# Kernel optimization log

Measured on AMD Instinct MI355X. Metric: run time of the kernel, lower is better.

Reference implementation:

```python
import jax, jax.numpy as jnp
import numpy as np

N_NODES = 100000
N_EDGES = 400000
IN_DIM, HID, OUT_DIM, NUM_REL = 768, 256, 128, 3


def _init_linear(key, fan_in, fan_out):
    k1, k2 = jax.random.split(key)
    s = 1.0 / np.sqrt(fan_in)
    W = jax.random.uniform(k1, (fan_in, fan_out), jnp.float32, -s, s)
    b = jax.random.uniform(k2, (fan_out,), jnp.float32, -s, s)
    return W, b


def setup_inputs() -> dict:
    key = jax.random.key(0)
    ks = jax.random.split(key, 12)
    x = jax.random.normal(ks[0], (N_NODES, IN_DIM), jnp.float32)
    edge_index = jax.random.randint(ks[1], (2, N_EDGES), 0, N_NODES, jnp.int64 if jax.config.jax_enable_x64 else jnp.int32).astype(jnp.int32)
    edge_type = jax.random.randint(ks[2], (N_EDGES,), 0, NUM_REL).astype(jnp.int32)
    W1, b1 = _init_linear(ks[3], IN_DIM, HID)
    s = 1.0 / np.sqrt(HID)
    conv1_W = jax.random.uniform(ks[4], (NUM_REL, HID, HID), jnp.float32, -s, s)
    conv1_root = jax.random.uniform(ks[5], (HID, HID), jnp.float32, -s, s)
    conv1_bias = jnp.zeros((HID,), jnp.float32)
    conv2_W = jax.random.uniform(ks[6], (NUM_REL, HID, HID), jnp.float32, -s, s)
    conv2_root = jax.random.uniform(ks[7], (HID, HID), jnp.float32, -s, s)
    conv2_bias = jnp.zeros((HID,), jnp.float32)
    W2, b2 = _init_linear(ks[8], HID, OUT_DIM)
    Wc, bc = _init_linear(ks[9], OUT_DIM, 2)
    return {"x": x, "edge_index": edge_index, "edge_type": edge_type,
            "batch_size": 1024,
            "W1": W1, "b1": b1,
            "conv1_W": conv1_W, "conv1_root": conv1_root, "conv1_bias": conv1_bias,
            "conv2_W": conv2_W, "conv2_root": conv2_root, "conv2_bias": conv2_bias,
            "W2": W2, "b2": b2, "Wc": Wc, "bc": bc}


def rgcn_conv(h, src, dst, edge_type, W, root, bias):
    # PyG RGCNConv: mean aggregation per relation + root transform + bias
    n = h.shape[0]
    hs = h[src]                                   # [E, HID] gather
    out = h @ root + bias                         # root/self term
    for r in range(NUM_REL):                      # fixed small relation count
        w = (edge_type == r).astype(h.dtype)      # [E]
        msg = (hs @ W[r]) * w[:, None]            # per-relation transform
        ssum = jax.ops.segment_sum(msg, dst, num_segments=n)
        cnt = jax.ops.segment_sum(w, dst, num_segments=n)
        out = out + ssum / jnp.maximum(cnt, 1.0)[:, None]
    return out


def reference(x, edge_index, edge_type, batch_size,
              W1, b1, conv1_W, conv1_root, conv1_bias,
              conv2_W, conv2_root, conv2_bias, W2, b2, Wc, bc):
    src, dst = edge_index[0], edge_index[1]
    h = jax.nn.relu(x @ W1 + b1)                  # linear1 + ReLU
    h = rgcn_conv(h, src, dst, edge_type, conv1_W, conv1_root, conv1_bias)
    # dropout: identity at inference
    h = rgcn_conv(h, src, dst, edge_type, conv2_W, conv2_root, conv2_bias)
    h = jax.nn.relu(h @ W2 + b2)                  # linear2 + ReLU
    logits = h @ Wc + bc                          # classifier
    return logits[:batch_size]
```

## Files before the change

### kernel.cpp

```cpp
#include <hip/hip_runtime.h>


#define N_NODES 100000
#define N_EDGES 400000
#define IN_DIM  768
#define HID     256
#define OUT_DIM 128
#define NREL    3
#define BATCH   1024
#define KCAT    1024
#define MSGW    768
#define CAP0    32768
#define CAP1    8192
#define ECAP1   32768
#define ECAP2   8192

typedef __attribute__((ext_vector_type(8))) short bf16x8;
typedef __attribute__((ext_vector_type(4))) float f32x4;

static __device__ __forceinline__ int imin(int a, int b) { return a < b ? a : b; }

static __device__ __forceinline__ unsigned short f2bf(float f) {
    union { float f; unsigned int u; } v; v.f = f;
    unsigned int r = v.u + 0x7FFFu + ((v.u >> 16) & 1u);
    return (unsigned short)(r >> 16);
}

__global__ __launch_bounds__(256) void zero_prep(
    uint4* __restrict__ zp, int nz,
    const float* __restrict__ W1,
    const float* __restrict__ c1root, const float* __restrict__ c1W,
    const float* __restrict__ c2root, const float* __restrict__ c2W,
    unsigned short* __restrict__ w1s,
    unsigned short* __restrict__ B1s,
    unsigned short* __restrict__ B2s)
{
    int t = blockIdx.x * blockDim.x + threadIdx.x;
    if (t < nz) { zp[t] = make_uint4(0u, 0u, 0u, 0u); return; }
    int u = t - nz;
    const int P1 = (IN_DIM * HID) / 8;
    const int P2 = (KCAT * HID) / 8;
    unsigned int pk[4];
    if (u < P1) {
        int base = u * 8;
        int j0 = base & 31, c = (base >> 5) & 255, s = base >> 13;
        #pragma unroll
        for (int q = 0; q < 4; q++) {
            unsigned short lo = f2bf(W1[((s * 32 + j0 + 2 * q) << 8) + c]);
            unsigned short hi = f2bf(W1[((s * 32 + j0 + 2 * q + 1) << 8) + c]);
            pk[q] = (unsigned int)lo | ((unsigned int)hi << 16);
        }
        *(uint4*)&w1s[base] = make_uint4(pk[0], pk[1], pk[2], pk[3]);
    } else if (u < P1 + 2 * P2) {
        int which2 = (u - P1) >= P2;
        const float* root = which2 ? c2root : c1root;
        const float* Wr   = which2 ? c2W : c1W;
        unsigned short* dst = which2 ? B2s : B1s;
        int base = ((u - P1) - (which2 ? P2 : 0)) * 8;
        int j0 = base & 31, c = (base >> 5) & 255, s = base >> 13;
        int k0 = s * 32 + j0;
        #pragma unroll
        for (int q = 0; q < 4; q++) {
            int ka = k0 + 2 * q, kb = ka + 1;
            float va = (ka < HID) ? root[(ka << 8) + c] : Wr[((ka - HID) << 8) + c];
            float vb = (kb < HID) ? root[(kb << 8) + c] : Wr[((kb - HID) << 8) + c];
            pk[q] = (unsigned int)f2bf(va) | ((unsigned int)f2bf(vb) << 16);
        }
        *(uint4*)&dst[base] = make_uint4(pk[0], pk[1], pk[2], pk[3]);
    }
}


__global__ void mark1c(const int* __restrict__ ei, int* __restrict__ need1,
                       int* __restrict__ elist2, int* __restrict__ ectr2) {
    int e = blockIdx.x * blockDim.x + threadIdx.x;
    if (e >= N_EDGES) return;
    if (ei[N_EDGES + e] < BATCH) {
        need1[ei[e]] = 1;
        int p = atomicAdd(ectr2, 1);
        if (p < ECAP2) elist2[p] = e;
    }
}

__global__ void mark0c(const int* __restrict__ ei, const int* __restrict__ need1,
                       int* __restrict__ need0,
                       int* __restrict__ elist1, int* __restrict__ ectr1) {
    int e = blockIdx.x * blockDim.x + threadIdx.x;
    if (e >= N_EDGES) return;
    int d = ei[N_EDGES + e];
    if (d < BATCH || need1[d]) {
        need0[ei[e]] = 1;
        int p = atomicAdd(ectr1, 1);
        if (p < ECAP1) elist1[p] = e;
    }
}

__global__ void compact_both(const int* __restrict__ need1, const int* __restrict__ need0,
                             int* __restrict__ idx1, int* __restrict__ map1, int* __restrict__ n1ctr,
                             int* __restrict__ idx0, int* __restrict__ map0, int* __restrict__ n0ctr) {
    int i = blockIdx.x * blockDim.x + threadIdx.x;
    if (i >= N_NODES) return;
    int f1 = (i < BATCH) | need1[i];
    int f0 = f1 | need0[i];
    if (f1) {
        int p = atomicAdd(n1ctr, 1);
        if (p < CAP1) { idx1[p] = i; map1[i] = p; } else map1[i] = -1;
    } else map1[i] = -1;
    if (f0) {
        int p = atomicAdd(n0ctr, 1);
        if (p < CAP0) { idx0[p] = i; map0[i] = p; } else map0[i] = -1;
    } else map0[i] = -1;
}

__global__ void scatter_c(const int* __restrict__ ei, const int* __restrict__ et,
                          const int* __restrict__ elist, const int* __restrict__ ectr, int ecap,
                          const int* __restrict__ mapSrc, const int* __restrict__ mapDst,
                          const float* __restrict__ hsrc,
                          float* __restrict__ Amsg, float* __restrict__ cnt,
                          int cntStride) {
    int g = blockIdx.x * blockDim.x + threadIdx.x;
    int ii = g >> 6, lane = g & 63;
    int n = imin(*ectr, ecap);
    if (ii >= n) return;
    int e = elist[ii];
    int d = ei[N_EDGES + e];
    int row = mapDst ? mapDst[d] : d;
    if (row < 0) return;
    int s = mapSrc[ei[e]];
    if (s < 0) return;
    int r = et[e];
    float4 v = *(const float4*)(hsrc + (size_t)s * HID + lane * 4);
    float* dp = Amsg + (size_t)row * MSGW + (size_t)r * HID + lane * 4;
    atomicAdd(dp + 0, v.x);
    atomicAdd(dp + 1, v.y);
    atomicAdd(dp + 2, v.z);
    atomicAdd(dp + 3, v.w);
    if (lane == 0) atomicAdd(cnt + (size_t)r * cntStride + row, 1.0f);
}

__global__ __launch_bounds__(256) void gemm1_mfma(
    const float* __restrict__ x, const int* __restrict__ idx0,
    const unsigned short* __restrict__ w1s, const float* __restrict__ b1,
    float* __restrict__ h0c, const int* __restrict__ Mptr, int Mcap)
{
    int M = imin(*Mptr, Mcap);
    int bm = blockIdx.x * 64;
    if (bm >= M) return;

    __shared__ unsigned short As[64][40];
    __shared__ unsigned short Bs[256][40];

    int tid = threadIdx.x;
    int w = tid >> 6, lane = tid & 63;
    int l16 = lane & 15, lhi = lane >> 4;

    int ar = tid >> 2, ac = tid & 3;
    int gr = idx0[imin(bm + ar, M - 1)];
    const float* aptr = x + (size_t)gr * IN_DIM + ac * 8;

    f32x4 acc[16];
    #pragma unroll
    for (int i = 0; i < 16; i++) acc[i] = (f32x4)0.0f;

    for (int k0 = 0; k0 < IN_DIM; k0 += 32) {
        float4 a0 = *(const float4*)(aptr + k0);
        float4 a1 = *(const float4*)(aptr + k0 + 4);
        unsigned int p0 = (unsigned int)f2bf(a0.x) | ((unsigned int)f2bf(a0.y) << 16);
        unsigned int p1 = (unsigned int)f2bf(a0.z) | ((unsigned int)f2bf(a0.w) << 16);
        unsigned int p2 = (unsigned int)f2bf(a1.x) | ((unsigned int)f2bf(a1.y) << 16);
        unsigned int p3 = (unsigned int)f2bf(a1.z) | ((unsigned int)f2bf(a1.w) << 16);
        *(uint4*)&As[ar][ac * 8] = make_uint4(p0, p1, p2, p3);

        const uint4* bsrc = (const uint4*)(w1s + ((size_t)(k0 >> 5) * 256 + tid) * 32);
        int bswz = (tid >> 3) & 3;
        uint4 b0 = bsrc[0], b1v = bsrc[1], b2 = bsrc[2], b3 = bsrc[3];
        *(uint4*)&Bs[tid][(0 ^ bswz) * 8] = b0;
        *(uint4*)&Bs[tid][(1 ^ bswz) * 8] = b1v;
        *(uint4*)&Bs[tid][(2 ^ bswz) * 8] = b2;
        *(uint4*)&Bs[tid][(3 ^ bswz) * 8] = b3;
        __syncthreads();

        bf16x8 af = *(bf16x8*)&As[w * 16 + l16][lhi * 8];
        #pragma unroll
        for (int f = 0; f < 16; f++) {
            int col = f * 16 + l16;
            bf16x8 bf = *(bf16x8*)&Bs[col][(lhi ^ ((col >> 3) & 3)) * 8];
            acc[f] = __builtin_amdgcn_mfma_f32_16x16x32_bf16(af, bf, acc[f], 0, 0, 0);
        }
        __syncthreads();
    }

    #pragma unroll
    for (int f = 0; f < 16; f++) {
        int col = f * 16 + l16;
        float bb = b1[col];
        #pragma unroll
        for (int reg = 0; reg < 4; reg++) {
            int row = bm + w * 16 + lhi * 4 + reg;
            if (row < M) h0c[(size_t)row * HID + col] = fmaxf(acc[f][reg] + bb, 0.0f);
        }
    }
}

__global__ __launch_bounds__(256) void conv_mfma(
    const float* __restrict__ hsrc,
    const int* __restrict__ idx, const int* __restrict__ map,
    const float* __restrict__ Amsg,
    const float* __restrict__ cnt, int cntStride,
    const unsigned short* __restrict__ Bt, const float* __restrict__ bias,
    float* __restrict__ Cout, const int* __restrict__ Mptr, int Mcap)
{
    int M = Mptr ? imin(*Mptr, Mcap) : Mcap;
    int bm = blockIdx.x * 64;
    if (bm >= M) return;

    __shared__ unsigned short As[64][40];
    __shared__ unsigned short Bs[256][40];

    int tid = threadIdx.x;
    int w = tid >> 6, lane = tid & 63;
    int l16 = lane & 15, lhi = lane >> 4;

    int ar = tid >> 2, ac = tid & 3;
    int row = imin(bm + ar, M - 1);
    int node = idx ? idx[row] : row;
    int grow = map[node]; if (grow < 0) grow = 0;
    const float* rootp = hsrc + (size_t)grow * HID + ac * 8;
    const float* msgp  = Amsg + (size_t)row * MSGW + ac * 8;
    float sc[NREL];
    #pragma unroll
    for (int r = 0; r < NREL; r++)
        sc[r] = 1.0f / fmaxf(cnt[(size_t)r * cntStride + row], 1.0f);

    f32x4 acc[16];
    #pragma unroll
    for (int i = 0; i < 16; i++) acc[i] = (f32x4)0.0f;

    for (int k0 = 0; k0 < KCAT; k0 += 32) {
        float4 a0, a1;
        if (k0 < HID) {
            a0 = *(const float4*)(rootp + k0);
            a1 = *(const float4*)(rootp + k0 + 4);
        } else {
            float s = sc[(k0 - HID) >> 8];
            a0 = *(const float4*)(msgp + (k0 - HID));
            a1 = *(const float4*)(msgp + (k0 - HID) + 4);
            a0.x *= s; a0.y *= s; a0.z *= s; a0.w *= s;
            a1.x *= s; a1.y *= s; a1.z *= s; a1.w *= s;
        }
        unsigned int p0 = (unsigned int)f2bf(a0.x) | ((unsigned int)f2bf(a0.y) << 16);
        unsigned int p1 = (unsigned int)f2bf(a0.z) | ((unsigned int)f2bf(a0.w) << 16);
        unsigned int p2 = (unsigned int)f2bf(a1.x) | ((unsigned int)f2bf(a1.y) << 16);
        unsigned int p3 = (unsigned int)f2bf(a1.z) | ((unsigned int)f2bf(a1.w) << 16);
        *(uint4*)&As[ar][ac * 8] = make_uint4(p0, p1, p2, p3);

        const uint4* bsrc = (const uint4*)(Bt + ((size_t)(k0 >> 5) * 256 + tid) * 32);
        int bswz = (tid >> 3) & 3;
        uint4 b0 = bsrc[0], b1v = bsrc[1], b2 = bsrc[2], b3 = bsrc[3];
        *(uint4*)&Bs[tid][(0 ^ bswz) * 8] = b0;
        *(uint4*)&Bs[tid][(1 ^ bswz) * 8] = b1v;
        *(uint4*)&Bs[tid][(2 ^ bswz) * 8] = b2;
        *(uint4*)&Bs[tid][(3 ^ bswz) * 8] = b3;
        __syncthreads();

        bf16x8 af = *(bf16x8*)&As[w * 16 + l16][lhi * 8];
        #pragma unroll
        for (int f = 0; f < 16; f++) {
            int col = f * 16 + l16;
            bf16x8 bf = *(bf16x8*)&Bs[col][(lhi ^ ((col >> 3) & 3)) * 8];
            acc[f] = __builtin_amdgcn_mfma_f32_16x16x32_bf16(af, bf, acc[f], 0, 0, 0);
        }
        __syncthreads();
    }

    #pragma unroll
    for (int f = 0; f < 16; f++) {
        int col = f * 16 + l16;
        float bb = bias[col];
        #pragma unroll
        for (int reg = 0; reg < 4; reg++) {
            int r = bm + w * 16 + lhi * 4 + reg;
            if (r < M) Cout[(size_t)r * HID + col] = acc[f][reg] + bb;
        }
    }
}

__global__ __launch_bounds__(256) void lin2_cls(
    const float* __restrict__ h2, const float* __restrict__ W2,
    const float* __restrict__ b2, const float* __restrict__ Wc,
    const float* __restrict__ bc, float* __restrict__ out)
{
    __shared__ float As[16][36];
    __shared__ float Bs[16][132];

    int tid = threadIdx.x;
    int bm = blockIdx.x * 32;
    int tx = tid & 15, ty = tid >> 4;
    int brow = tid >> 4, bch = tid & 15;

    float acc[2][8] = {};

    for (int k0 = 0; k0 < HID; k0 += 16) {
        if (tid < 128) {
            int arow = tid >> 2, ach = tid & 3;
            float4 av = *(const float4*)(h2 + (size_t)(bm + arow) * HID + k0 + ach * 4);
            As[ach * 4 + 0][arow] = av.x;
            As[ach * 4 + 1][arow] = av.y;
            As[ach * 4 + 2][arow] = av.z;
            As[ach * 4 + 3][arow] = av.w;
        }
        const float* bp = W2 + (size_t)(k0 + brow) * OUT_DIM;
        *(float4*)&Bs[brow][bch * 4]      = *(const float4*)(bp + bch * 4);
        *(float4*)&Bs[brow][64 + bch * 4] = *(const float4*)(bp + 64 + bch * 4);
        __syncthreads();
        #pragma unroll
        for (int k = 0; k < 16; k++) {
            float a0 = As[k][ty * 2], a1 = As[k][ty * 2 + 1];
            float4 b0 = *(const float4*)&Bs[k][tx * 8];
            float4 b1 = *(const float4*)&Bs[k][tx * 8 + 4];
            acc[0][0] += a0 * b0.x; acc[0][1] += a0 * b0.y; acc[0][2] += a0 * b0.z; acc[0][3] += a0 * b0.w;
            acc[0][4] += a0 * b1.x; acc[0][5] += a0 * b1.y; acc[0][6] += a0 * b1.z; acc[0][7] += a0 * b1.w;
            acc[1][0] += a1 * b0.x; acc[1][1] += a1 * b0.y; acc[1][2] += a1 * b0.z; acc[1][3] += a1 * b0.w;
            acc[1][4] += a1 * b1.x; acc[1][5] += a1 * b1.y; acc[1][6] += a1 * b1.z; acc[1][7] += a1 * b1.w;
        }
        __syncthreads();
    }

    float s0[2] = {0.f, 0.f}, s1[2] = {0.f, 0.f};
    #pragma unroll
    for (int j = 0; j < 8; j++) {
        int col = tx * 8 + j;
        float w0 = Wc[col * 2 + 0], w1 = Wc[col * 2 + 1];
        float bb = b2[col];
        #pragma unroll
        for (int i = 0; i < 2; i++) {
            float h = fmaxf(acc[i][j] + bb, 0.0f);
            s0[i] += h * w0;
            s1[i] += h * w1;
        }
    }
    #pragma unroll
    for (int o = 1; o <= 8; o <<= 1) {
        #pragma unroll
        for (int i = 0; i < 2; i++) {
            s0[i] += __shfl_xor(s0[i], o);
            s1[i] += __shfl_xor(s1[i], o);
        }
    }
    if (tx == 0) {
        #pragma unroll
        for (int i = 0; i < 2; i++) {
            int row = bm + ty * 2 + i;
            out[row * 2 + 0] = s0[i] + bc[0];
            out[row * 2 + 1] = s1[i] + bc[1];
        }
    }
}


extern "C" void kernel_launch(void* const* d_in, const int* in_sizes, int n_in,
                              void* d_out, int out_size, void* d_ws, size_t ws_size,
                              hipStream_t stream) {
    const float* x      = (const float*)d_in[0];
    const int*   ei     = (const int*)d_in[1];
    const int*   et     = (const int*)d_in[2];
    const float* W1     = (const float*)d_in[4];
    const float* b1     = (const float*)d_in[5];
    const float* c1W    = (const float*)d_in[6];
    const float* c1root = (const float*)d_in[7];
    const float* c1bias = (const float*)d_in[8];
    const float* c2W    = (const float*)d_in[9];
    const float* c2root = (const float*)d_in[10];
    const float* c2bias = (const float*)d_in[11];
    const float* W2     = (const float*)d_in[12];
    const float* b2     = (const float*)d_in[13];
    const float* Wc     = (const float*)d_in[14];
    const float* bc     = (const float*)d_in[15];
    float* out = (float*)d_out;

    char* ws = (char*)d_ws;
    size_t off = 0;
    auto alloc = [&](size_t bytes) -> char* {
        char* p = ws + off;
        off = (off + bytes + 255) & ~(size_t)255;
        return p;
    };

    size_t zb_ctr   = 16;
    size_t zb_cnt1  = (size_t)NREL * CAP1 * 4;
    size_t zb_cnt2  = (size_t)NREL * BATCH * 4;
    size_t zb_need  = (size_t)N_NODES * 4;
    size_t zb_amsg1 = (size_t)CAP1 * MSGW * 4;
    size_t zb_amsg2 = (size_t)BATCH * MSGW * 4;
    size_t zbytes = zb_ctr + zb_cnt1 + zb_cnt2 + 2 * zb_need + zb_amsg1 + zb_amsg2;
    char* zblock = alloc(zbytes);
    int*   n1ctr = (int*)zblock;
    int*   n0ctr = n1ctr + 1;
    int*   ectr1 = n1ctr + 2;
    int*   ectr2 = n1ctr + 3;
    float* cnt1  = (float*)(zblock + zb_ctr);
    float* cnt2  = (float*)(zblock + zb_ctr + zb_cnt1);
    int*   need1 = (int*)(zblock + zb_ctr + zb_cnt1 + zb_cnt2);
    int*   need0 = (int*)((char*)need1 + zb_need);
    float* Amsg1 = (float*)((char*)need0 + zb_need);
    float* Amsg2 = (float*)((char*)Amsg1 + zb_amsg1);

    int* map1  = (int*)alloc(N_NODES * 4);
    int* map0  = (int*)alloc(N_NODES * 4);
    int* idx1  = (int*)alloc(CAP1 * 4);
    int* idx0  = (int*)alloc(CAP0 * 4);
    int* elist1 = (int*)alloc(ECAP1 * 4);
    int* elist2 = (int*)alloc(ECAP2 * 4);
    float* h0c = (float*)alloc((size_t)CAP0 * HID * 4);
    float* h1c = (float*)alloc((size_t)CAP1 * HID * 4);
    float* h2  = (float*)alloc((size_t)BATCH * HID * 4);
    unsigned short* w1s = (unsigned short*)alloc((size_t)IN_DIM * HID * 2);
    unsigned short* B1s = (unsigned short*)alloc((size_t)KCAT * HID * 2);
    unsigned short* B2s = (unsigned short*)alloc((size_t)KCAT * HID * 2);
    (void)ws_size; (void)in_sizes; (void)n_in; (void)out_size;

    const int NB = 256;
    dim3 nodeGrid((N_NODES + NB - 1) / NB);
    dim3 edgeGrid((N_EDGES + NB - 1) / NB);

    int nz = (int)((zbytes + 15) / 16);
    int prep_threads = (IN_DIM * HID) / 8 + 2 * (KCAT * HID) / 8;
    int zp_total = nz + prep_threads;

    zero_prep<<<dim3((zp_total + NB - 1) / NB), NB, 0, stream>>>(
        (uint4*)zblock, nz, W1, c1root, c1W, c2root, c2W, w1s, B1s, B2s);
    mark1c<<<edgeGrid, NB, 0, stream>>>(ei, need1, elist2, ectr2);
    mark0c<<<edgeGrid, NB, 0, stream>>>(ei, need1, need0, elist1, ectr1);
    compact_both<<<nodeGrid, NB, 0, stream>>>(need1, need0, idx1, map1, n1ctr, idx0, map0, n0ctr);
    gemm1_mfma<<<dim3(CAP0 / 64), NB, 0, stream>>>(x, idx0, w1s, b1, h0c, n0ctr, CAP0);
    scatter_c<<<dim3(ECAP1 * 64 / NB), NB, 0, stream>>>(ei, et, elist1, ectr1, ECAP1,
                                                        map0, map1, h0c, Amsg1, cnt1, CAP1);
    conv_mfma<<<dim3(CAP1 / 64), NB, 0, stream>>>(h0c, idx1, map0, Amsg1, cnt1, CAP1,
                                                  B1s, c1bias, h1c, n1ctr, CAP1);
    scatter_c<<<dim3(ECAP2 * 64 / NB), NB, 0, stream>>>(ei, et, elist2, ectr2, ECAP2,
                                                        map1, nullptr, h1c, Amsg2, cnt2, BATCH);
    conv_mfma<<<dim3(BATCH / 64), NB, 0, stream>>>(h1c, nullptr, map1, Amsg2, cnt2, BATCH,
                                                   B2s, c2bias, h2, nullptr, BATCH);
    lin2_cls<<<dim3(BATCH / 32), NB, 0, stream>>>(h2, W2, b2, Wc, bc, out);
}
```

Measured before the change: 408.6 us.

## Prepack weights in MFMA fragment order and drop LDS staging in GEMMs

Weight matrices are reordered during prep into the per-lane MFMA 16x16x32 fragment layout, so GEMM kernels load B fragments directly from global memory. A fragments are likewise loaded and converted per lane, and the shared-memory tiles and block barriers are removed. This trades LDS traffic and synchronization for redundant per-wave global/L2 reads of the weights.

```diff
diff --git a/kernel.cpp b/kernel.cpp
--- a/kernel.cpp
+++ b/kernel.cpp
@@ -26,47 +26,58 @@
     return (unsigned short)(r >> 16);
 }
 
+static __device__ __forceinline__ bf16x8 pack8(float4 a0, float4 a1) {
+    union { uint4 u; bf16x8 v; } c;
+    c.u.x = (unsigned int)f2bf(a0.x) | ((unsigned int)f2bf(a0.y) << 16);
+    c.u.y = (unsigned int)f2bf(a0.z) | ((unsigned int)f2bf(a0.w) << 16);
+    c.u.z = (unsigned int)f2bf(a1.x) | ((unsigned int)f2bf(a1.y) << 16);
+    c.u.w = (unsigned int)f2bf(a1.z) | ((unsigned int)f2bf(a1.w) << 16);
+    return c.v;
+}
+
+#define NP1 ((IN_DIM * HID) / 8)
+#define NP2 ((KCAT * HID) / 8)
+
 __global__ __launch_bounds__(256) void zero_prep(
     uint4* __restrict__ zp, int nz,
     const float* __restrict__ W1,
     const float* __restrict__ c1root, const float* __restrict__ c1W,
     const float* __restrict__ c2root, const float* __restrict__ c2W,
-    unsigned short* __restrict__ w1s,
-    unsigned short* __restrict__ B1s,
-    unsigned short* __restrict__ B2s)
+    unsigned short* __restrict__ w1t,
+    unsigned short* __restrict__ B1t,
+    unsigned short* __restrict__ B2t)
 {
     int t = blockIdx.x * blockDim.x + threadIdx.x;
     if (t < nz) { zp[t] = make_uint4(0u, 0u, 0u, 0u); return; }
     int u = t - nz;
-    const int P1 = (IN_DIM * HID) / 8;
-    const int P2 = (KCAT * HID) / 8;
-    unsigned int pk[4];
-    if (u < P1) {
-        int base = u * 8;
-        int j0 = base & 31, c = (base >> 5) & 255, s = base >> 13;
-        #pragma unroll
-        for (int q = 0; q < 4; q++) {
-            unsigned short lo = f2bf(W1[((s * 32 + j0 + 2 * q) << 8) + c]);
-            unsigned short hi = f2bf(W1[((s * 32 + j0 + 2 * q + 1) << 8) + c]);
-            pk[q] = (unsigned int)lo | ((unsigned int)hi << 16);
-        }
-        *(uint4*)&w1s[base] = make_uint4(pk[0], pk[1], pk[2], pk[3]);
-    } else if (u < P1 + 2 * P2) {
-        int which2 = (u - P1) >= P2;
+    if (u < NP1) {
+        int s = u >> 10, f = (u >> 6) & 15, l = u & 63;
+        int kb = s * 32 + ((l >> 4) << 3);
+        int c  = (f << 4) + (l & 15);
+        const float* src = W1 + (size_t)kb * HID + c;
+        unsigned int p0 = (unsigned int)f2bf(src[0])       | ((unsigned int)f2bf(src[HID])     << 16);
+        unsigned int p1 = (unsigned int)f2bf(src[2 * HID]) | ((unsigned int)f2bf(src[3 * HID]) << 16);
+        unsigned int p2 = (unsigned int)f2bf(src[4 * HID]) | ((unsigned int)f2bf(src[5 * HID]) << 16);
+        unsigned int p3 = (unsigned int)f2bf(src[6 * HID]) | ((unsigned int)f2bf(src[7 * HID]) << 16);
+        *(uint4*)&w1t[(size_t)u * 8] = make_uint4(p0, p1, p2, p3);
+    } else if (u < NP1 + 2 * NP2) {
+        int which2 = (u - NP1) >= NP2;
+        int v = (u - NP1) - (which2 ? NP2 : 0);
         const float* root = which2 ? c2root : c1root;
         const float* Wr   = which2 ? c2W : c1W;
-        unsigned short* dst = which2 ? B2s : B1s;
-        int base = ((u - P1) - (which2 ? P2 : 0)) * 8;
-        int j0 = base & 31, c = (base >> 5) & 255, s = base >> 13;
-        int k0 = s * 32 + j0;
+        unsigned short* dst = which2 ? B2t : B1t;
+        int s = v >> 10, f = (v >> 6) & 15, l = v & 63;
+        int kb = s * 32 + ((l >> 4) << 3);
+        int c  = (f << 4) + (l & 15);
+        unsigned int pk[4];
         #pragma unroll
         for (int q = 0; q < 4; q++) {
-            int ka = k0 + 2 * q, kb = ka + 1;
-            float va = (ka < HID) ? root[(ka << 8) + c] : Wr[((ka - HID) << 8) + c];
-            float vb = (kb < HID) ? root[(kb << 8) + c] : Wr[((kb - HID) << 8) + c];
+            int ka = kb + 2 * q, kbq = ka + 1;
+            float va = (ka  < HID) ? root[(size_t)ka  * HID + c] : Wr[(size_t)(ka  - HID) * HID + c];
+            float vb = (kbq < HID) ? root[(size_t)kbq * HID + c] : Wr[(size_t)(kbq - HID) * HID + c];
             pk[q] = (unsigned int)f2bf(va) | ((unsigned int)f2bf(vb) << 16);
         }
-        *(uint4*)&dst[base] = make_uint4(pk[0], pk[1], pk[2], pk[3]);
+        *(uint4*)&dst[(size_t)v * 8] = make_uint4(pk[0], pk[1], pk[2], pk[3]);
     }
 }
 
@@ -111,6 +122,7 @@
         if (p < CAP0) { idx0[p] = i; map0[i] = p; } else map0[i] = -1;
     } else map0[i] = -1;
 }
+
 
 __global__ void scatter_c(const int* __restrict__ ei, const int* __restrict__ et,
                           const int* __restrict__ elist, const int* __restrict__ ectr, int ecap,
@@ -140,54 +152,34 @@
 
 __global__ __launch_bounds__(256) void gemm1_mfma(
     const float* __restrict__ x, const int* __restrict__ idx0,
-    const unsigned short* __restrict__ w1s, const float* __restrict__ b1,
+    const unsigned short* __restrict__ w1t, const float* __restrict__ b1,
     float* __restrict__ h0c, const int* __restrict__ Mptr, int Mcap)
 {
     int M = imin(*Mptr, Mcap);
     int bm = blockIdx.x * 64;
     if (bm >= M) return;
 
-    __shared__ unsigned short As[64][40];
-    __shared__ unsigned short Bs[256][40];
-
     int tid = threadIdx.x;
-    int w = tid >> 6, lane = tid & 63;
-    int l16 = lane & 15, lhi = lane >> 4;
-
-    int ar = tid >> 2, ac = tid & 3;
-    int gr = idx0[imin(bm + ar, M - 1)];
-    const float* aptr = x + (size_t)gr * IN_DIM + ac * 8;
+    int w = tid >> 6, l = tid & 63;
+    int l16 = l & 15, lhi = l >> 4;
+
+    int gr = idx0[imin(bm + w * 16 + l16, M - 1)];
+    const float* ap = x + (size_t)gr * IN_DIM + lhi * 8;
 
     f32x4 acc[16];
     #pragma unroll
     for (int i = 0; i < 16; i++) acc[i] = (f32x4)0.0f;
 
-    for (int k0 = 0; k0 < IN_DIM; k0 += 32) {
-        float4 a0 = *(const float4*)(aptr + k0);
-        float4 a1 = *(const float4*)(aptr + k0 + 4);
-        unsigned int p0 = (unsigned int)f2bf(a0.x) | ((unsigned int)f2bf(a0.y) << 16);
-        unsigned int p1 = (unsigned int)f2bf(a0.z) | ((unsigned int)f2bf(a0.w) << 16);
-        unsigned int p2 = (unsigned int)f2bf(a1.x) | ((unsigned int)f2bf(a1.y) << 16);
-        unsigned int p3 = (unsigned int)f2bf(a1.z) | ((unsigned int)f2bf(a1.w) << 16);
-        *(uint4*)&As[ar][ac * 8] = make_uint4(p0, p1, p2, p3);
-
-        const uint4* bsrc = (const uint4*)(w1s + ((size_t)(k0 >> 5) * 256 + tid) * 32);
-        int bswz = (tid >> 3) & 3;
-        uint4 b0 = bsrc[0], b1v = bsrc[1], b2 = bsrc[2], b3 = bsrc[3];
-        *(uint4*)&Bs[tid][(0 ^ bswz) * 8] = b0;
-        *(uint4*)&Bs[tid][(1 ^ bswz) * 8] = b1v;
-        *(uint4*)&Bs[tid][(2 ^ bswz) * 8] = b2;
-        *(uint4*)&Bs[tid][(3 ^ bswz) * 8] = b3;
-        __syncthreads();
-
-        bf16x8 af = *(bf16x8*)&As[w * 16 + l16][lhi * 8];
+    for (int s = 0; s < IN_DIM / 32; s++) {
+        float4 a0 = *(const float4*)(ap + s * 32);
+        float4 a1 = *(const float4*)(ap + s * 32 + 4);
+        bf16x8 af = pack8(a0, a1);
+        const unsigned short* base = w1t + ((size_t)(s * 16) * 64 + l) * 8;
         #pragma unroll
         for (int f = 0; f < 16; f++) {
-            int col = f * 16 + l16;
-            bf16x8 bf = *(bf16x8*)&Bs[col][(lhi ^ ((col >> 3) & 3)) * 8];
+            bf16x8 bf = *(const bf16x8*)(base + (size_t)f * 512);
             acc[f] = __builtin_amdgcn_mfma_f32_16x16x32_bf16(af, bf, acc[f], 0, 0, 0);
         }
-        __syncthreads();
     }
 
     #pragma unroll
@@ -214,63 +206,46 @@
     int bm = blockIdx.x * 64;
     if (bm >= M) return;
 
-    __shared__ unsigned short As[64][40];
-    __shared__ unsigned short Bs[256][40];
-
     int tid = threadIdx.x;
-    int w = tid >> 6, lane = tid & 63;
-    int l16 = lane & 15, lhi = lane >> 4;
-
-    int ar = tid >> 2, ac = tid & 3;
-    int row = imin(bm + ar, M - 1);
+    int w = tid >> 6, l = tid & 63;
+    int l16 = l & 15, lhi = l >> 4;
+
+    int row = imin(bm + w * 16 + l16, M - 1);
     int node = idx ? idx[row] : row;
     int grow = map[node]; if (grow < 0) grow = 0;
-    const float* rootp = hsrc + (size_t)grow * HID + ac * 8;
-    const float* msgp  = Amsg + (size_t)row * MSGW + ac * 8;
+    const float* rootp = hsrc + (size_t)grow * HID;
+    const float* msgp  = Amsg + (size_t)row * MSGW;
     float sc[NREL];
     #pragma unroll
     for (int r = 0; r < NREL; r++)
         sc[r] = 1.0f / fmaxf(cnt[(size_t)r * cntStride + row], 1.0f);
 
+    int kb = lhi * 8;
+
     f32x4 acc[16];
     #pragma unroll
     for (int i = 0; i < 16; i++) acc[i] = (f32x4)0.0f;
 
-    for (int k0 = 0; k0 < KCAT; k0 += 32) {
+    for (int s = 0; s < KCAT / 32; s++) {
+        int k0 = s * 32 + kb;
         float4 a0, a1;
         if (k0 < HID) {
             a0 = *(const float4*)(rootp + k0);
             a1 = *(const float4*)(rootp + k0 + 4);
         } else {
-            float s = sc[(k0 - HID) >> 8];
+            float sf = sc[(k0 - HID) >> 8];
             a0 = *(const float4*)(msgp + (k0 - HID));
             a1 = *(const float4*)(msgp + (k0 - HID) + 4);
-            a0.x *= s; a0.y *= s; a0.z *= s; a0.w *= s;
-            a1.x *= s; a1.y *= s; a1.z *= s; a1.w *= s;
-        }
-        unsigned int p0 = (unsigned int)f2bf(a0.x) | ((unsigned int)f2bf(a0.y) << 16);
-        unsigned int p1 = (unsigned int)f2bf(a0.z) | ((unsigned int)f2bf(a0.w) << 16);
-        unsigned int p2 = (unsigned int)f2bf(a1.x) | ((unsigned int)f2bf(a1.y) << 16);
-        unsigned int p3 = (unsigned int)f2bf(a1.z) | ((unsigned int)f2bf(a1.w) << 16);
-        *(uint4*)&As[ar][ac * 8] = make_uint4(p0, p1, p2, p3);
-
-        const uint4* bsrc = (const uint4*)(Bt + ((size_t)(k0 >> 5) * 256 + tid) * 32);
-        int bswz = (tid >> 3) & 3;
-        uint4 b0 = bsrc[0], b1v = bsrc[1], b2 = bsrc[2], b3 = bsrc[3];
-        *(uint4*)&Bs[tid][(0 ^ bswz) * 8] = b0;
-        *(uint4*)&Bs[tid][(1 ^ bswz) * 8] = b1v;
-        *(uint4*)&Bs[tid][(2 ^ bswz) * 8] = b2;
-        *(uint4*)&Bs[tid][(3 ^ bswz) * 8] = b3;
-        __syncthreads();
-
-        bf16x8 af = *(bf16x8*)&As[w * 16 + l16][lhi * 8];
+            a0.x *= sf; a0.y *= sf; a0.z *= sf; a0.w *= sf;
+            a1.x *= sf; a1.y *= sf; a1.z *= sf; a1.w *= sf;
+        }
+        bf16x8 af = pack8(a0, a1);
+        const unsigned short* base = Bt + ((size_t)(s * 16) * 64 + l) * 8;
         #pragma unroll
         for (int f = 0; f < 16; f++) {
-            int col = f * 16 + l16;
-            bf16x8 bf = *(bf16x8*)&Bs[col][(lhi ^ ((col >> 3) & 3)) * 8];
+            bf16x8 bf = *(const bf16x8*)(base + (size_t)f * 512);
             acc[f] = __builtin_amdgcn_mfma_f32_16x16x32_bf16(af, bf, acc[f], 0, 0, 0);
         }
-        __syncthreads();
     }
 
     #pragma unroll
@@ -414,9 +389,9 @@
     float* h0c = (float*)alloc((size_t)CAP0 * HID * 4);
     float* h1c = (float*)alloc((size_t)CAP1 * HID * 4);
     float* h2  = (float*)alloc((size_t)BATCH * HID * 4);
-    unsigned short* w1s = (unsigned short*)alloc((size_t)IN_DIM * HID * 2);
-    unsigned short* B1s = (unsigned short*)alloc((size_t)KCAT * HID * 2);
-    unsigned short* B2s = (unsigned short*)alloc((size_t)KCAT * HID * 2);
+    unsigned short* w1t = (unsigned short*)alloc((size_t)IN_DIM * HID * 2);
+    unsigned short* B1t = (unsigned short*)alloc((size_t)KCAT * HID * 2);
+    unsigned short* B2t = (unsigned short*)alloc((size_t)KCAT * HID * 2);
     (void)ws_size; (void)in_sizes; (void)n_in; (void)out_size;
 
     const int NB = 256;
@@ -424,22 +399,21 @@
     dim3 edgeGrid((N_EDGES + NB - 1) / NB);
 
     int nz = (int)((zbytes + 15) / 16);
-    int prep_threads = (IN_DIM * HID) / 8 + 2 * (KCAT * HID) / 8;
-    int zp_total = nz + prep_threads;
+    int zp_total = nz + NP1 + 2 * NP2;
 
     zero_prep<<<dim3((zp_total + NB - 1) / NB), NB, 0, stream>>>(
-        (uint4*)zblock, nz, W1, c1root, c1W, c2root, c2W, w1s, B1s, B2s);
+        (uint4*)zblock, nz, W1, c1root, c1W, c2root, c2W, w1t, B1t, B2t);
     mark1c<<<edgeGrid, NB, 0, stream>>>(ei, need1, elist2, ectr2);
     mark0c<<<edgeGrid, NB, 0, stream>>>(ei, need1, need0, elist1, ectr1);
     compact_both<<<nodeGrid, NB, 0, stream>>>(need1, need0, idx1, map1, n1ctr, idx0, map0, n0ctr);
-    gemm1_mfma<<<dim3(CAP0 / 64), NB, 0, stream>>>(x, idx0, w1s, b1, h0c, n0ctr, CAP0);
+    gemm1_mfma<<<dim3(CAP0 / 64), NB, 0, stream>>>(x, idx0, w1t, b1, h0c, n0ctr, CAP0);
     scatter_c<<<dim3(ECAP1 * 64 / NB), NB, 0, stream>>>(ei, et, elist1, ectr1, ECAP1,
                                                         map0, map1, h0c, Amsg1, cnt1, CAP1);
     conv_mfma<<<dim3(CAP1 / 64), NB, 0, stream>>>(h0c, idx1, map0, Amsg1, cnt1, CAP1,
-                                                  B1s, c1bias, h1c, n1ctr, CAP1);
+                                                  B1t, c1bias, h1c, n1ctr, CAP1);
     scatter_c<<<dim3(ECAP2 * 64 / NB), NB, 0, stream>>>(ei, et, elist2, ectr2, ECAP2,
                                                         map1, nullptr, h1c, Amsg2, cnt2, BATCH);
     conv_mfma<<<dim3(BATCH / 64), NB, 0, stream>>>(h1c, nullptr, map1, Amsg2, cnt2, BATCH,
-                                                   B2s, c2bias, h2, nullptr, BATCH);
+                                                   B2t, c2bias, h2, nullptr, BATCH);
     lin2_cls<<<dim3(BATCH / 32), NB, 0, stream>>>(h2, W2, b2, Wc, bc, out);
 }
```

Measured after the change: 467.1 us. 14.3% more time.

## Fuse launch chain: merge mark with prep, fuse conv2 with lin2 classifier via MFMA

Applied to the files above, without the earlier changes.

Cuts the launch count by folding the mark1 edge pass into the weight-prep/zero kernel, merging mark0 with the compact1 node pass, and splitting compaction so compact0 reads map1. The small counters and need arrays are now cleared with hipMemsetAsync ahead of those kernels. The second conv GEMM is fused with linear2 and the classifier: h2 stays in LDS as bf16, and a bf16 MFMA with a pre-swizzled W2 replaces the fp32 lin2 kernel. This removes launch overhead and the h2 round trip through global memory, at the cost of bf16 rounding in linear2.

```diff
diff --git a/kernel.cpp b/kernel.cpp
--- a/kernel.cpp
+++ b/kernel.cpp
@@ -26,24 +26,30 @@
     return (unsigned short)(r >> 16);
 }
 
-__global__ __launch_bounds__(256) void zero_prep(
-    uint4* __restrict__ zp, int nz,
+#define P1n  ((IN_DIM * HID) / 8)
+#define P2n  ((KCAT * HID) / 8)
+#define PW2n ((HID * OUT_DIM) / 8)
+
+__global__ __launch_bounds__(256) void prep_mark1(
+    uint4* __restrict__ zp, int nzA,
     const float* __restrict__ W1,
     const float* __restrict__ c1root, const float* __restrict__ c1W,
     const float* __restrict__ c2root, const float* __restrict__ c2W,
+    const float* __restrict__ W2,
     unsigned short* __restrict__ w1s,
     unsigned short* __restrict__ B1s,
-    unsigned short* __restrict__ B2s)
+    unsigned short* __restrict__ B2s,
+    unsigned short* __restrict__ W2t,
+    const int* __restrict__ ei, int* __restrict__ need1,
+    int* __restrict__ elist2, int* __restrict__ ectr2)
 {
     int t = blockIdx.x * blockDim.x + threadIdx.x;
-    if (t < nz) { zp[t] = make_uint4(0u, 0u, 0u, 0u); return; }
-    int u = t - nz;
-    const int P1 = (IN_DIM * HID) / 8;
-    const int P2 = (KCAT * HID) / 8;
-    unsigned int pk[4];
-    if (u < P1) {
+    if (t < nzA) { zp[t] = make_uint4(0u, 0u, 0u, 0u); return; }
+    int u = t - nzA;
+    if (u < P1n) {
         int base = u * 8;
         int j0 = base & 31, c = (base >> 5) & 255, s = base >> 13;
+        unsigned int pk[4];
         #pragma unroll
         for (int q = 0; q < 4; q++) {
             unsigned short lo = f2bf(W1[((s * 32 + j0 + 2 * q) << 8) + c]);
@@ -51,14 +57,18 @@
             pk[q] = (unsigned int)lo | ((unsigned int)hi << 16);
         }
         *(uint4*)&w1s[base] = make_uint4(pk[0], pk[1], pk[2], pk[3]);
-    } else if (u < P1 + 2 * P2) {
-        int which2 = (u - P1) >= P2;
+        return;
+    }
+    u -= P1n;
+    if (u < 2 * P2n) {
+        int which2 = u >= P2n;
         const float* root = which2 ? c2root : c1root;
         const float* Wr   = which2 ? c2W : c1W;
         unsigned short* dst = which2 ? B2s : B1s;
-        int base = ((u - P1) - (which2 ? P2 : 0)) * 8;
+        int base = (u - (which2 ? P2n : 0)) * 8;
         int j0 = base & 31, c = (base >> 5) & 255, s = base >> 13;
         int k0 = s * 32 + j0;
+        unsigned int pk[4];
         #pragma unroll
         for (int q = 0; q < 4; q++) {
             int ka = k0 + 2 * q, kb = ka + 1;
@@ -67,46 +77,63 @@
             pk[q] = (unsigned int)f2bf(va) | ((unsigned int)f2bf(vb) << 16);
         }
         *(uint4*)&dst[base] = make_uint4(pk[0], pk[1], pk[2], pk[3]);
-    }
-}
-
-
-__global__ void mark1c(const int* __restrict__ ei, int* __restrict__ need1,
-                       int* __restrict__ elist2, int* __restrict__ ectr2) {
-    int e = blockIdx.x * blockDim.x + threadIdx.x;
-    if (e >= N_EDGES) return;
-    if (ei[N_EDGES + e] < BATCH) {
-        need1[ei[e]] = 1;
-        int p = atomicAdd(ectr2, 1);
-        if (p < ECAP2) elist2[p] = e;
-    }
-}
-
-__global__ void mark0c(const int* __restrict__ ei, const int* __restrict__ need1,
-                       int* __restrict__ need0,
-                       int* __restrict__ elist1, int* __restrict__ ectr1) {
-    int e = blockIdx.x * blockDim.x + threadIdx.x;
-    if (e >= N_EDGES) return;
-    int d = ei[N_EDGES + e];
-    if (d < BATCH || need1[d]) {
-        need0[ei[e]] = 1;
-        int p = atomicAdd(ectr1, 1);
-        if (p < ECAP1) elist1[p] = e;
-    }
-}
-
-__global__ void compact_both(const int* __restrict__ need1, const int* __restrict__ need0,
-                             int* __restrict__ idx1, int* __restrict__ map1, int* __restrict__ n1ctr,
-                             int* __restrict__ idx0, int* __restrict__ map0, int* __restrict__ n0ctr) {
+        return;
+    }
+    u -= 2 * P2n;
+    if (u < PW2n) {
+        int s = u >> 9, f = (u >> 6) & 7, l = u & 63;
+        int kb = s * 32 + ((l >> 4) << 3);
+        int c  = (f << 4) + (l & 15);
+        unsigned int pk[4];
+        #pragma unroll
+        for (int q = 0; q < 4; q++) {
+            unsigned short lo = f2bf(W2[(size_t)(kb + 2 * q)     * OUT_DIM + c]);
+            unsigned short hi = f2bf(W2[(size_t)(kb + 2 * q + 1) * OUT_DIM + c]);
+            pk[q] = (unsigned int)lo | ((unsigned int)hi << 16);
+        }
+        *(uint4*)&W2t[(size_t)u * 8] = make_uint4(pk[0], pk[1], pk[2], pk[3]);
+        return;
+    }
+    u -= PW2n;
+    if (u < N_EDGES) {
+        if (ei[N_EDGES + u] < BATCH) {
+            need1[ei[u]] = 1;
+            int p = atomicAdd(ectr2, 1);
+            if (p < ECAP2) elist2[p] = u;
+        }
+    }
+}
+
+__global__ void mark0_compact1(const int* __restrict__ ei, const int* __restrict__ need1,
+                               int* __restrict__ need0,
+                               int* __restrict__ elist1, int* __restrict__ ectr1,
+                               int* __restrict__ idx1, int* __restrict__ map1,
+                               int* __restrict__ n1ctr) {
+    int t = blockIdx.x * blockDim.x + threadIdx.x;
+    if (t < N_EDGES) {
+        int d = ei[N_EDGES + t];
+        if (d < BATCH || need1[d]) {
+            need0[ei[t]] = 1;
+            int p = atomicAdd(ectr1, 1);
+            if (p < ECAP1) elist1[p] = t;
+        }
+        return;
+    }
+    int i = t - N_EDGES;
+    if (i < N_NODES) {
+        if ((i < BATCH) | need1[i]) {
+            int p = atomicAdd(n1ctr, 1);
+            if (p < CAP1) { idx1[p] = i; map1[i] = p; } else map1[i] = -1;
+        } else map1[i] = -1;
+    }
+}
+
+__global__ void compact0(const int* __restrict__ map1, const int* __restrict__ need0,
+                         int* __restrict__ idx0, int* __restrict__ map0,
+                         int* __restrict__ n0ctr) {
     int i = blockIdx.x * blockDim.x + threadIdx.x;
     if (i >= N_NODES) return;
-    int f1 = (i < BATCH) | need1[i];
-    int f0 = f1 | need0[i];
-    if (f1) {
-        int p = atomicAdd(n1ctr, 1);
-        if (p < CAP1) { idx1[p] = i; map1[i] = p; } else map1[i] = -1;
-    } else map1[i] = -1;
-    if (f0) {
+    if ((map1[i] >= 0) | need0[i]) {
         int p = atomicAdd(n0ctr, 1);
         if (p < CAP0) { idx0[p] = i; map0[i] = p; } else map0[i] = -1;
     } else map0[i] = -1;
@@ -285,74 +312,124 @@
     }
 }
 
-__global__ __launch_bounds__(256) void lin2_cls(
-    const float* __restrict__ h2, const float* __restrict__ W2,
-    const float* __restrict__ b2, const float* __restrict__ Wc,
-    const float* __restrict__ bc, float* __restrict__ out)
+__global__ __launch_bounds__(256) void conv2_fused(
+    const float* __restrict__ hsrc, const int* __restrict__ map,
+    const float* __restrict__ Amsg, const float* __restrict__ cnt,
+    const unsigned short* __restrict__ Bt, const float* __restrict__ c2bias,
+    const unsigned short* __restrict__ W2t, const float* __restrict__ b2,
+    const float* __restrict__ Wc, const float* __restrict__ bc,
+    float* __restrict__ out)
 {
-    __shared__ float As[16][36];
-    __shared__ float Bs[16][132];
+    int bm = blockIdx.x * 64;
+
+    __shared__ unsigned short As[64][40];
+    __shared__ unsigned short Bs[256][40];
+    __shared__ unsigned short h2s[64][264];
 
     int tid = threadIdx.x;
-    int bm = blockIdx.x * 32;
-    int tx = tid & 15, ty = tid >> 4;
-    int brow = tid >> 4, bch = tid & 15;
-
-    float acc[2][8] = {};
-
-    for (int k0 = 0; k0 < HID; k0 += 16) {
-        if (tid < 128) {
-            int arow = tid >> 2, ach = tid & 3;
-            float4 av = *(const float4*)(h2 + (size_t)(bm + arow) * HID + k0 + ach * 4);
-            As[ach * 4 + 0][arow] = av.x;
-            As[ach * 4 + 1][arow] = av.y;
-            As[ach * 4 + 2][arow] = av.z;
-            As[ach * 4 + 3][arow] = av.w;
-        }
-        const float* bp = W2 + (size_t)(k0 + brow) * OUT_DIM;
-        *(float4*)&Bs[brow][bch * 4]      = *(const float4*)(bp + bch * 4);
-        *(float4*)&Bs[brow][64 + bch * 4] = *(const float4*)(bp + 64 + bch * 4);
+    int w = tid >> 6, lane = tid & 63;
+    int l16 = lane & 15, lhi = lane >> 4;
+
+    int ar = tid >> 2, ac = tid & 3;
+    int row = bm + ar;
+    int grow = map[row]; if (grow < 0) grow = 0;
+    const float* rootp = hsrc + (size_t)grow * HID + ac * 8;
+    const float* msgp  = Amsg + (size_t)row * MSGW + ac * 8;
+    float sc[NREL];
+    #pragma unroll
+    for (int r = 0; r < NREL; r++)
+        sc[r] = 1.0f / fmaxf(cnt[(size_t)r * BATCH + row], 1.0f);
+
+    f32x4 acc[16];
+    #pragma unroll
+    for (int i = 0; i < 16; i++) acc[i] = (f32x4)0.0f;
+
+    for (int k0 = 0; k0 < KCAT; k0 += 32) {
+        float4 a0, a1;
+        if (k0 < HID) {
+            a0 = *(const float4*)(rootp + k0);
+            a1 = *(const float4*)(rootp + k0 + 4);
+        } else {
+            float s = sc[(k0 - HID) >> 8];
+            a0 = *(const float4*)(msgp + (k0 - HID));
+            a1 = *(const float4*)(msgp + (k0 - HID) + 4);
+            a0.x *= s; a0.y *= s; a0.z *= s; a0.w *= s;
+            a1.x *= s; a1.y *= s; a1.z *= s; a1.w *= s;
+        }
+        unsigned int p0 = (unsigned int)f2bf(a0.x) | ((unsigned int)f2bf(a0.y) << 16);
+        unsigned int p1 = (unsigned int)f2bf(a0.z) | ((unsigned int)f2bf(a0.w) << 16);
+        unsigned int p2 = (unsigned int)f2bf(a1.x) | ((unsigned int)f2bf(a1.y) << 16);
+        unsigned int p3 = (unsigned int)f2bf(a1.z) | ((unsigned int)f2bf(a1.w) << 16);
+        *(uint4*)&As[ar][ac * 8] = make_uint4(p0, p1, p2, p3);
+
+        const uint4* bsrc = (const uint4*)(Bt + ((size_t)(k0 >> 5) * 256 + tid) * 32);
+        int bswz = (tid >> 3) & 3;
+        uint4 b0 = bsrc[0], b1v = bsrc[1], b2v = bsrc[2], b3 = bsrc[3];
+        *(uint4*)&Bs[tid][(0 ^ bswz) * 8] = b0;
+        *(uint4*)&Bs[tid][(1 ^ bswz) * 8] = b1v;
+        *(uint4*)&Bs[tid][(2 ^ bswz) * 8] = b2v;
+        *(uint4*)&Bs[tid][(3 ^ bswz) * 8] = b3;
         __syncthreads();
-        #pragma unroll
-        for (int k = 0; k < 16; k++) {
-            float a0 = As[k][ty * 2], a1 = As[k][ty * 2 + 1];
-            float4 b0 = *(const float4*)&Bs[k][tx * 8];
-            float4 b1 = *(const float4*)&Bs[k][tx * 8 + 4];
-            acc[0][0] += a0 * b0.x; acc[0][1] += a0 * b0.y; acc[0][2] += a0 * b0.z; acc[0][3] += a0 * b0.w;
-            acc[0][4] += a0 * b1.x; acc[0][5] += a0 * b1.y; acc[0][6] += a0 * b1.z; acc[0][7] += a0 * b1.w;
-            acc[1][0] += a1 * b0.x; acc[1][1] += a1 * b0.y; acc[1][2] += a1 * b0.z; acc[1][3] += a1 * b0.w;
-            acc[1][4] += a1 * b1.x; acc[1][5] += a1 * b1.y; acc[1][6] += a1 * b1.z; acc[1][7] += a1 * b1.w;
+
+        bf16x8 af = *(bf16x8*)&As[w * 16 + l16][lhi * 8];
+        #pragma unroll
+        for (int f = 0; f < 16; f++) {
+            int col = f * 16 + l16;
+            bf16x8 bf = *(bf16x8*)&Bs[col][(lhi ^ ((col >> 3) & 3)) * 8];
+            acc[f] = __builtin_amdgcn_mfma_f32_16x16x32_bf16(af, bf, acc[f], 0, 0, 0);
         }
         __syncthreads();
     }
 
-    float s0[2] = {0.f, 0.f}, s1[2] = {0.f, 0.f};
-    #pragma unroll
-    for (int j = 0; j < 8; j++) {
-        int col = tx * 8 + j;
+    #pragma unroll
+    for (int f = 0; f < 16; f++) {
+        int col = f * 16 + l16;
+        float bb = c2bias[col];
+        #pragma unroll
+        for (int reg = 0; reg < 4; reg++)
+            h2s[w * 16 + lhi * 4 + reg][col] = f2bf(acc[f][reg] + bb);
+    }
+    __syncthreads();
+
+    f32x4 acc2[8];
+    #pragma unroll
+    for (int i = 0; i < 8; i++) acc2[i] = (f32x4)0.0f;
+    for (int s = 0; s < 8; s++) {
+        bf16x8 af = *(bf16x8*)&h2s[w * 16 + l16][s * 32 + lhi * 8];
+        #pragma unroll
+        for (int f = 0; f < 8; f++) {
+            bf16x8 bf = *(const bf16x8*)(W2t + ((size_t)(s * 8 + f) * 64 + lane) * 8);
+            acc2[f] = __builtin_amdgcn_mfma_f32_16x16x32_bf16(af, bf, acc2[f], 0, 0, 0);
+        }
+    }
+
+    float p0[4] = {0.f, 0.f, 0.f, 0.f}, p1[4] = {0.f, 0.f, 0.f, 0.f};
+    #pragma unroll
+    for (int f = 0; f < 8; f++) {
+        int col = f * 16 + l16;
         float w0 = Wc[col * 2 + 0], w1 = Wc[col * 2 + 1];
         float bb = b2[col];
         #pragma unroll
-        for (int i = 0; i < 2; i++) {
-            float h = fmaxf(acc[i][j] + bb, 0.0f);
-            s0[i] += h * w0;
-            s1[i] += h * w1;
+        for (int reg = 0; reg < 4; reg++) {
+            float h = fmaxf(acc2[f][reg] + bb, 0.0f);
+            p0[reg] += h * w0;
+            p1[reg] += h * w1;
         }
     }
     #pragma unroll
     for (int o = 1; o <= 8; o <<= 1) {
         #pragma unroll
-        for (int i = 0; i < 2; i++) {
-            s0[i] += __shfl_xor(s0[i], o);
-            s1[i] += __shfl_xor(s1[i], o);
-        }
-    }
-    if (tx == 0) {
-        #pragma unroll
-        for (int i = 0; i < 2; i++) {
-            int row = bm + ty * 2 + i;
-            out[row * 2 + 0] = s0[i] + bc[0];
-            out[row * 2 + 1] = s1[i] + bc[1];
+        for (int reg = 0; reg < 4; reg++) {
+            p0[reg] += __shfl_xor(p0[reg], o);
+            p1[reg] += __shfl_xor(p1[reg], o);
+        }
+    }
+    if (l16 == 0) {
+        #pragma unroll
+        for (int reg = 0; reg < 4; reg++) {
+            int r = bm + w * 16 + lhi * 4 + reg;
+            out[r * 2 + 0] = p0[reg] + bc[0];
+            out[r * 2 + 1] = p1[reg] + bc[1];
         }
     }
 }
@@ -386,24 +463,27 @@
         return p;
     };
 
-    size_t zb_ctr   = 16;
-    size_t zb_cnt1  = (size_t)NREL * CAP1 * 4;
-    size_t zb_cnt2  = (size_t)NREL * BATCH * 4;
-    size_t zb_need  = (size_t)N_NODES * 4;
-    size_t zb_amsg1 = (size_t)CAP1 * MSGW * 4;
-    size_t zb_amsg2 = (size_t)BATCH * MSGW * 4;
-    size_t zbytes = zb_ctr + zb_cnt1 + zb_cnt2 + 2 * zb_need + zb_amsg1 + zb_amsg2;
-    char* zblock = alloc(zbytes);
-    int*   n1ctr = (int*)zblock;
+    size_t zb_ctr  = 16;
+    size_t zb_cnt1 = (size_t)NREL * CAP1 * 4;
+    size_t zb_cnt2 = (size_t)NREL * BATCH * 4;
+    size_t zb_need = (size_t)N_NODES * 4;
+    size_t msbytes = zb_ctr + zb_cnt1 + zb_cnt2 + 2 * zb_need;
+    char* zsmall = alloc(msbytes);
+    int*   n1ctr = (int*)zsmall;
     int*   n0ctr = n1ctr + 1;
     int*   ectr1 = n1ctr + 2;
     int*   ectr2 = n1ctr + 3;
-    float* cnt1  = (float*)(zblock + zb_ctr);
-    float* cnt2  = (float*)(zblock + zb_ctr + zb_cnt1);
-    int*   need1 = (int*)(zblock + zb_ctr + zb_cnt1 + zb_cnt2);
+    float* cnt1  = (float*)(zsmall + zb_ctr);
+    float* cnt2  = (float*)(zsmall + zb_ctr + zb_cnt1);
+    int*   need1 = (int*)(zsmall + zb_ctr + zb_cnt1 + zb_cnt2);
     int*   need0 = (int*)((char*)need1 + zb_need);
-    float* Amsg1 = (float*)((char*)need0 + zb_need);
-    float* Amsg2 = (float*)((char*)Amsg1 + zb_amsg1);
+
+    size_t zb_amsg1 = (size_t)CAP1 * MSGW * 4;
+    size_t zb_amsg2 = (size_t)BATCH * MSGW * 4;
+    char* amsg = alloc(zb_amsg1 + zb_amsg2);
+    float* Amsg1 = (float*)amsg;
+    float* Amsg2 = (float*)(amsg + zb_amsg1);
+    int nzA = (int)((zb_amsg1 + zb_amsg2) / 16);
 
     int* map1  = (int*)alloc(N_NODES * 4);
     int* map0  = (int*)alloc(N_NODES * 4);
@@ -413,25 +493,23 @@
     int* elist2 = (int*)alloc(ECAP2 * 4);
     float* h0c = (float*)alloc((size_t)CAP0 * HID * 4);
     float* h1c = (float*)alloc((size_t)CAP1 * HID * 4);
-    float* h2  = (float*)alloc((size_t)BATCH * HID * 4);
     unsigned short* w1s = (unsigned short*)alloc((size_t)IN_DIM * HID * 2);
     unsigned short* B1s = (unsigned short*)alloc((size_t)KCAT * HID * 2);
     unsigned short* B2s = (unsigned short*)alloc((size_t)KCAT * HID * 2);
+    unsigned short* W2t = (unsigned short*)alloc((size_t)HID * OUT_DIM * 2);
     (void)ws_size; (void)in_sizes; (void)n_in; (void)out_size;
 
     const int NB = 256;
-    dim3 nodeGrid((N_NODES + NB - 1) / NB);
-    dim3 edgeGrid((N_EDGES + NB - 1) / NB);
-
-    int nz = (int)((zbytes + 15) / 16);
-    int prep_threads = (IN_DIM * HID) / 8 + 2 * (KCAT * HID) / 8;
-    int zp_total = nz + prep_threads;
-
-    zero_prep<<<dim3((zp_total + NB - 1) / NB), NB, 0, stream>>>(
-        (uint4*)zblock, nz, W1, c1root, c1W, c2root, c2W, w1s, B1s, B2s);
-    mark1c<<<edgeGrid, NB, 0, stream>>>(ei, need1, elist2, ectr2);
-    mark0c<<<edgeGrid, NB, 0, stream>>>(ei, need1, need0, elist1, ectr1);
-    compact_both<<<nodeGrid, NB, 0, stream>>>(need1, need0, idx1, map1, n1ctr, idx0, map0, n0ctr);
+
+    hipMemsetAsync(zsmall, 0, msbytes, stream);
+    int n1_total = nzA + P1n + 2 * P2n + PW2n + N_EDGES;
+    prep_mark1<<<dim3((n1_total + NB - 1) / NB), NB, 0, stream>>>(
+        (uint4*)amsg, nzA, W1, c1root, c1W, c2root, c2W, W2,
+        w1s, B1s, B2s, W2t, ei, need1, elist2, ectr2);
+    int n2_total = N_EDGES + N_NODES;
+    mark0_compact1<<<dim3((n2_total + NB - 1) / NB), NB, 0, stream>>>(
+        ei, need1, need0, elist1, ectr1, idx1, map1, n1ctr);
+    compact0<<<dim3((N_NODES + NB - 1) / NB), NB, 0, stream>>>(map1, need0, idx0, map0, n0ctr);
     gemm1_mfma<<<dim3(CAP0 / 64), NB, 0, stream>>>(x, idx0, w1s, b1, h0c, n0ctr, CAP0);
     scatter_c<<<dim3(ECAP1 * 64 / NB), NB, 0, stream>>>(ei, et, elist1, ectr1, ECAP1,
                                                         map0, map1, h0c, Amsg1, cnt1, CAP1);
@@ -439,7 +517,6 @@
                                                   B1s, c1bias, h1c, n1ctr, CAP1);
     scatter_c<<<dim3(ECAP2 * 64 / NB), NB, 0, stream>>>(ei, et, elist2, ectr2, ECAP2,
                                                         map1, nullptr, h1c, Amsg2, cnt2, BATCH);
-    conv_mfma<<<dim3(BATCH / 64), NB, 0, stream>>>(h1c, nullptr, map1, Amsg2, cnt2, BATCH,
-                                                   B2s, c2bias, h2, nullptr, BATCH);
-    lin2_cls<<<dim3(BATCH / 32), NB, 0, stream>>>(h2, W2, b2, Wc, bc, out);
-}
+    conv2_fused<<<dim3(BATCH / 64), NB, 0, stream>>>(h1c, map1, Amsg2, cnt2,
+                                                     B2s, c2bias, W2t, b2, Wc, bc, out);
+}
```

After: 379.4 us (median of 2 runs). -7.1%, faster.
